# Optimization experiments

Measured on AMD Instinct MI355X. Metric: run time of the kernel, lower is better.

## Reference

```python
import jax, jax.numpy as jnp
import numpy as np

B, Q, NCLS1, C = 8, 900, 11, 256
NUM_ANCHOR = 100
H, W = 200, 200


def _make_view(b):
    # maps homogeneous (x0, y0, x1, y1, 1) box coords (meters-ish) to BEV pixels:
    # pixel = 20 * coord + 100  (keeps random boxes inside the 200x200 grid)
    v = np.zeros((5, 5), dtype=np.float32)
    for i in range(4):
        v[i, i] = 20.0
        v[i, 4] = 100.0
    v[4, 4] = 1.0
    return jnp.asarray(np.broadcast_to(v, (b, 5, 5)).copy())


def setup_inputs() -> dict:
    key = jax.random.key(0)
    k1, k2, k3 = jax.random.split(key, 3)
    return {
        "pred_boxes": jax.random.normal(k1, (B, Q, 4), dtype=jnp.float32),
        "pred_logits": jax.random.normal(k2, (B, Q, NCLS1), dtype=jnp.float32),
        "box_feats": jax.random.normal(k3, (B, Q, C), dtype=jnp.float32),
        "view": _make_view(B),
    }


def _box_to_bev(pred_boxes, pred_logits, box_feats, view):
    # scores = max over non-background classes of softmax(logits)
    scores = jnp.max(jax.nn.softmax(pred_logits, axis=-1)[..., :-1], axis=-1)  # [b,Q]
    _, idx = jax.lax.top_k(scores, NUM_ANCHOR)                                 # [b,N]

    boxes = jnp.take_along_axis(pred_boxes, idx[:, :, None], axis=1)[..., :4]  # [b,N,4]
    feats = jnp.take_along_axis(box_feats, idx[:, :, None], axis=1)            # [b,N,C]

    cx, cy = boxes[..., 0], boxes[..., 1]
    w, h = jnp.exp(boxes[..., 2]), jnp.exp(boxes[..., 3])
    xyxy = jnp.stack([cx - 0.5 * w, cy - 0.5 * h, cx + 0.5 * w, cy + 0.5 * h], axis=-1)
    xyxy1 = jnp.concatenate([xyxy, jnp.ones_like(xyxy[..., :1])], axis=-1)     # [b,N,5]

    coords = jnp.einsum("bij,bnj->bni", view, xyxy1)[..., :4].astype(jnp.int32)
    x0 = jnp.clip(coords[..., 0], 0, W)
    y0 = jnp.clip(coords[..., 1], 0, H)
    x1 = jnp.clip(coords[..., 2], 0, W)
    y1 = jnp.clip(coords[..., 3], 0, H)

    ys = jnp.arange(H, dtype=jnp.int32)
    xs = jnp.arange(W, dtype=jnp.int32)
    row = (ys[None, None, :] >= y0[:, :, None]) & (ys[None, None, :] < y1[:, :, None])  # [b,N,H]
    col = (xs[None, None, :] >= x0[:, :, None]) & (xs[None, None, :] < x1[:, :, None])  # [b,N,W]
    region = row[:, :, :, None] & col[:, :, None, :]                                    # [b,N,H,W]

    bev = jnp.einsum("bnhw,bnc->bhwc", region.astype(feats.dtype), feats)  # [b,H,W,C]
    mask = jnp.any(region, axis=1)                                          # [b,H,W]
    return bev, mask


def reference(pred_boxes, pred_logits, box_feats, view):
    return _box_to_bev(pred_boxes, pred_logits, box_feats, view)
```

## Files before the change

### kernel.cpp

```cpp
#include <hip/hip_runtime.h>
#include <math.h>

#define B_    8
#define Q_    900
#define NCLS_ 11
#define NANC_ 100
#define H_    200
#define W_    200
#define C_    256
#define HHALF 100
#define CHNK_ 113
#define CHEV_ 16

typedef float f32x4_ __attribute__((ext_vector_type(4)));

__global__ __launch_bounds__(128) void segdet_topk_kernel(
    const float* __restrict__ pred_boxes,
    const float* __restrict__ pred_logits,
    const float* __restrict__ view,
    int*  __restrict__ ws_idx,
    int4* __restrict__ ws_box)
{
    const int b     = blockIdx.x >> 3;
    const int chunk = blockIdx.x & 7;
    const int tid   = threadIdx.x;

    __shared__ __align__(16) float sc[Q_];

    for (int q2 = tid; q2 < Q_; q2 += 128) {
        const float* l = pred_logits + (b * Q_ + q2) * NCLS_;
        float v[NCLS_];
        float m = -INFINITY;
        #pragma unroll
        for (int i = 0; i < NCLS_; ++i) { v[i] = l[i]; m = fmaxf(m, v[i]); }
        float s = 0.0f, e10 = -INFINITY;
        #pragma unroll
        for (int i = 0; i < NCLS_; ++i) {
            float e = expf(v[i] - m);
            s += e;
            if (i < NCLS_ - 1) e10 = fmaxf(e10, e);
        }
        sc[q2] = e10 / s;
    }
    __syncthreads();

    const int q = chunk * CHNK_ + tid;
    if (tid < CHNK_ && q < Q_) {
        const float my = sc[q];
        int rank = 0;
        #pragma unroll 4
        for (int j4 = 0; j4 < Q_ / 4; ++j4) {
            const float4 o = *(const float4*)&sc[j4 * 4];
            const int j = j4 * 4;
            rank += (o.x > my) || (o.x == my && (j + 0) < q);
            rank += (o.y > my) || (o.y == my && (j + 1) < q);
            rank += (o.z > my) || (o.z == my && (j + 2) < q);
            rank += (o.w > my) || (o.w == my && (j + 3) < q);
        }
        if (rank < NANC_) {
            const float* bx = pred_boxes + (b * Q_ + q) * 4;
            double cx = (double)bx[0], cy = (double)bx[1];
            double w  = exp((double)bx[2]);
            double h  = exp((double)bx[3]);
            double p[5] = { cx - 0.5 * w, cy - 0.5 * h,
                            cx + 0.5 * w, cy + 0.5 * h, 1.0 };
            const float* v5 = view + b * 25;
            int ico[4];
            #pragma unroll
            for (int i = 0; i < 4; ++i) {
                double acc = 0.0;
                #pragma unroll
                for (int j = 0; j < 5; ++j) acc += (double)v5[i * 5 + j] * p[j];
                ico[i] = (int)acc;
            }
            int x0 = min(max(ico[0], 0), W_);
            int y0 = min(max(ico[1], 0), H_);
            int x1 = min(max(ico[2], 0), W_);
            int y1 = min(max(ico[3], 0), H_);
            const int slot = b * NANC_ + rank;
            ws_idx[slot] = q;
            ws_box[slot] = make_int4(x0, y0, x1, y1);
        }
    }
}

__device__ __forceinline__ void nt_store4(float* p, f32x4_ v) {
    __builtin_nontemporal_store(v, (f32x4_*)p);
}

__device__ __forceinline__ void gload_lds_16(const float* g, float* l) {
    __builtin_amdgcn_global_load_lds(
        (const __attribute__((address_space(1))) void*)g,
        (__attribute__((address_space(3))) void*)l,
        16, 0, 0);
}

__global__ __launch_bounds__(256) void segdet_bev_kernel(
    const float* __restrict__ box_feats,
    const int*   __restrict__ ws_idx,
    const int4*  __restrict__ ws_box,
    float* __restrict__ bev,
    float* __restrict__ mask)
{
    const int hidx = blockIdx.x / B_;
    const int b    = blockIdx.x % B_;
    const int h    = (hidx & 1) ? (HHALF - 1 - (hidx >> 1)) : (HHALF + (hidx >> 1));

    const int tid = threadIdx.x;
    const int ln  = tid & 63;
    const int wv  = tid >> 6;

    __shared__ __align__(16) float s_chunk[2][CHEV_ * C_];
    __shared__ int s_box[NANC_];
    __shared__ int s_nact;
    __shared__ int s_nopen[W_];
    __shared__ int s_ofs[W_ + 1];
    __shared__ int s_ent[2 * NANC_];
    __shared__ int s_wsum[4];

    if (tid < 64) {
        int na = 0;
        #pragma unroll
        for (int it = 0; it < 2; ++it) {
            int k = it * 64 + ln;
            bool act = false;
            int packed = 0;
            if (k < NANC_) {
                int4 bx = ws_box[b * NANC_ + k];
                int qi  = ws_idx[b * NANC_ + k];
                act = (bx.y <= h) && (h < bx.w) && (bx.x < bx.z);
                packed = bx.x | (bx.z << 8) | (qi << 16);
            }
            unsigned long long ball = __ballot(act);
            int pos = na + (int)__popcll(ball & ((1ull << ln) - 1ull));
            if (act) s_box[pos] = packed;
            na += (int)__popcll(ball);
        }
        if (ln == 0) s_nact = na;
    }
    __syncthreads();

    const int nact = s_nact;
    float* obase = bev + (size_t)(b * H_ + h) * W_ * C_ + ln * 4;
    float* mrow  = mask + (size_t)(b * H_ + h) * W_;

    if (nact == 0) {
        const f32x4_ z = {0.f, 0.f, 0.f, 0.f};
        for (int w = wv; w < W_; w += 4)
            nt_store4(obase + (size_t)w * C_, z);
        if (tid < W_) __builtin_nontemporal_store(0.0f, &mrow[tid]);
        return;
    }

    int ntot = 0;
    if (tid < W_) {
        int nopen = 0, nclose = 0, cov = 0;
        for (int k = 0; k < nact; ++k) {
            int pk = s_box[k];
            int x0 = pk & 0xFF, x1 = (pk >> 8) & 0xFF;
            nopen  += (x0 == tid);
            nclose += (x1 == tid);
            cov    += (x0 <= tid) && (tid < x1);
        }
        s_nopen[tid] = nopen;
        ntot = nopen + nclose;
        __builtin_nontemporal_store((cov > 0) ? 1.0f : 0.0f, &mrow[tid]);
    }

    int incl = ntot;
    #pragma unroll
    for (int d = 1; d < 64; d <<= 1) {
        int u = __shfl_up(incl, d);
        incl = (ln >= d) ? incl + u : incl;
    }
    if (ln == 63) s_wsum[wv] = incl;
    __syncthreads();

    int prev = 0;
    #pragma unroll
    for (int j = 0; j < 4; ++j) prev += (j < wv) ? s_wsum[j] : 0;
    const int ne = s_wsum[0] + s_wsum[1] + s_wsum[2] + s_wsum[3];
    if (tid < W_) s_ofs[tid] = prev + incl - ntot;
    if (tid == 0) s_ofs[W_] = ne;
    __syncthreads();

    if (tid < nact) {
        int pk = s_box[tid];
        int x0 = pk & 0xFF, x1 = (pk >> 8) & 0xFF, q = pk >> 16;
        int ro = 0, rc = 0;
        for (int j = 0; j < tid; ++j) {
            int pj = s_box[j];
            ro += ((pj & 0xFF) == x0);
            rc += (((pj >> 8) & 0xFF) == x1);
        }
        s_ent[s_ofs[x0] + ro] = q | (x0 << 10);
        if (x1 < W_)
            s_ent[s_ofs[x1] + s_nopen[x1] + rc] =
                (int)((unsigned)q | ((unsigned)x1 << 10) | 0x80000000u);
    }
    __syncthreads();

    const float* fbase = box_feats + (size_t)b * Q_ * C_ + ln * 4;
    const int nchunk = (ne + CHEV_ - 1) / CHEV_;

#define STAGE_(CI)                                                            \
    {                                                                         \
        const int base_ = (CI) * CHEV_;                                       \
        float* dst_ = &s_chunk[(CI) & 1][0];                                  \
        _Pragma("unroll")                                                     \
        for (int j = 0; j < 4; ++j) {                                         \
            const int e_ = base_ + wv * 4 + j;                                \
            if (e_ < ne) {                                                    \
                const int q_ = s_ent[e_] & 0x3FF;                             \
                gload_lds_16(fbase + (size_t)q_ * C_,                         \
                             dst_ + (wv * 4 + j) * C_);                       \
            }                                                                 \
        }                                                                     \
    }

    STAGE_(0);
    __syncthreads();

    f32x4_ acc = {0.f, 0.f, 0.f, 0.f};
    int cnt = 0;
    int w = wv;
    for (int ci = 0; ci < nchunk; ++ci) {
        if (ci + 1 < nchunk) STAGE_(ci + 1);
        const int ebeg = ci * CHEV_;
        const int eend = (ne < ebeg + CHEV_) ? ne : (ebeg + CHEV_);
        const float* cb = &s_chunk[ci & 1][0];
        for (int e = ebeg; e < eend; ++e) {
            const int ent = s_ent[e];
            const int pe  = (ent >> 10) & 0xFF;
            for (; w < pe; w += 4)
                nt_store4(obase + (size_t)w * C_, acc);
            const f32x4_ f = *(const f32x4_*)&cb[(e - ebeg) * C_ + ln * 4];
            if (ent < 0) { acc -= f; --cnt; }
            else         { acc += f; ++cnt; }
            if (cnt == 0) acc = (f32x4_){0.f, 0.f, 0.f, 0.f};
        }
        __syncthreads();
    }
#undef STAGE_
    for (; w < W_; w += 4)
        nt_store4(obase + (size_t)w * C_, acc);
}

extern "C" void kernel_launch(void* const* d_in, const int* in_sizes, int n_in,
                              void* d_out, int out_size, void* d_ws, size_t ws_size,
                              hipStream_t stream) {
    const float* pred_boxes  = (const float*)d_in[0];
    const float* pred_logits = (const float*)d_in[1];
    const float* box_feats   = (const float*)d_in[2];
    const float* view        = (const float*)d_in[3];

    float* bev  = (float*)d_out;
    float* mask = bev + (size_t)B_ * H_ * W_ * C_;

    int*  ws_idx = (int*)d_ws;
    int4* ws_box = (int4*)((char*)d_ws + 3200);

    segdet_topk_kernel<<<B_ * 8, 128, 0, stream>>>(pred_boxes, pred_logits, view,
                                                   ws_idx, ws_box);
    segdet_bev_kernel<<<B_ * H_, 256, 0, stream>>>(box_feats, ws_idx, ws_box,
                                                   bev, mask);
}
```

Measured before the change: 101.0 us.

## Split per-row event building into a separate prep kernel before BEV accumulation

```diff
diff --git a/kernel.cpp b/kernel.cpp
--- a/kernel.cpp
+++ b/kernel.cpp
@@ -11,6 +11,7 @@
 #define HHALF 100
 #define CHNK_ 113
 #define CHEV_ 16
+#define EVSTR_ 224
 
 typedef float f32x4_ __attribute__((ext_vector_type(4)));
 
@@ -95,6 +96,174 @@
         16, 0, 0);
 }
 
+__global__ __launch_bounds__(1024) void segdet_prep_kernel(
+    const int*  __restrict__ ws_idx,
+    const int4* __restrict__ ws_box,
+    int*  __restrict__ g_hdr,
+    int*  __restrict__ g_ev,
+    float* __restrict__ mask)
+{
+    const int sub = threadIdx.x >> 8;
+    const int t   = threadIdx.x & 255;
+    const int ln  = threadIdx.x & 63;
+    const int wv2 = (threadIdx.x >> 6) & 3;
+    const int rid = blockIdx.x * 4 + sub;
+    const int b   = rid / H_;
+    const int h   = rid % H_;
+
+    __shared__ __align__(16) int s_box[4][104];
+    __shared__ int s_na[4];
+    __shared__ int s_ws[4][4];
+
+    if (wv2 == 0) {
+        int na = 0;
+        #pragma unroll
+        for (int it = 0; it < 2; ++it) {
+            int k = it * 64 + ln;
+            bool act = false; int packed = 0;
+            if (k < NANC_) {
+                int4 bx = ws_box[b * NANC_ + k];
+                int qi  = ws_idx[b * NANC_ + k];
+                act = (bx.y <= h) && (h < bx.w) && (bx.x < bx.z);
+                packed = bx.x | (bx.z << 8) | (qi << 16);
+            }
+            unsigned long long ball = __ballot(act);
+            int pos = na + (int)__popcll(ball & ((1ull << ln) - 1ull));
+            if (act) s_box[sub][pos] = packed;
+            na += (int)__popcll(ball);
+        }
+        for (int idx = na + ln; idx < 104; idx += 64)
+            s_box[sub][idx] = 0xFFFF;
+        if (ln == 0) s_na[sub] = na;
+    }
+    __syncthreads();
+
+    const int nact = s_na[sub];
+    const int nk4  = (nact + 3) >> 2;
+
+    int nopen = 0, ncl = 0, cov = 0;
+#define CNT1_(PK) { const int x0_ = (PK) & 0xFF, x1_ = ((PK) >> 8) & 0xFF;    \
+        nopen += (x0_ == t); ncl += (x1_ == t);                               \
+        cov   += (x0_ <= t) && (t < x1_); }
+    if (t < W_) {
+        for (int k4 = 0; k4 < nk4; ++k4) {
+            const int4 p4 = *(const int4*)&s_box[sub][k4 * 4];
+            CNT1_(p4.x); CNT1_(p4.y); CNT1_(p4.z); CNT1_(p4.w);
+        }
+        mask[(size_t)rid * W_ + t] = (cov > 0) ? 1.0f : 0.0f;
+    }
+#undef CNT1_
+    const int ntot = nopen + ncl;
+
+    int incl = ntot;
+    #pragma unroll
+    for (int d = 1; d < 64; d <<= 1) {
+        int u = __shfl_up(incl, d);
+        incl = (ln >= d) ? incl + u : incl;
+    }
+    if (ln == 63) s_ws[sub][wv2] = incl;
+    __syncthreads();
+
+    int prev = 0;
+    #pragma unroll
+    for (int j = 0; j < 4; ++j) prev += (j < wv2) ? s_ws[sub][j] : 0;
+    const int ne  = s_ws[sub][0] + s_ws[sub][1] + s_ws[sub][2] + s_ws[sub][3];
+    const int ofs = prev + incl - ntot;
+    if (t == 0) g_hdr[rid] = ne;
+
+    if (t < W_ && ntot > 0) {
+        int po = ofs, pc = ofs + nopen;
+        int* dst = g_ev + (size_t)rid * EVSTR_;
+#define SCT1_(PK) { const int x0_ = (PK) & 0xFF, x1_ = ((PK) >> 8) & 0xFF;    \
+        const int q_ = (PK) >> 16;                                            \
+        if (x0_ == t) dst[po++] = q_ | (t << 10);                             \
+        if (x1_ == t) dst[pc++] = (int)((unsigned)q_ | ((unsigned)t << 10)    \
+                                         | 0x80000000u); }
+        for (int k4 = 0; k4 < nk4; ++k4) {
+            const int4 p4 = *(const int4*)&s_box[sub][k4 * 4];
+            SCT1_(p4.x); SCT1_(p4.y); SCT1_(p4.z); SCT1_(p4.w);
+        }
+#undef SCT1_
+    }
+}
+
+__global__ __launch_bounds__(256) void segdet_bev2_kernel(
+    const float* __restrict__ box_feats,
+    const int*   __restrict__ g_hdr,
+    const int*   __restrict__ g_ev,
+    float* __restrict__ bev)
+{
+    const int hidx = blockIdx.x / B_;
+    const int b    = blockIdx.x % B_;
+    const int h    = (hidx & 1) ? (HHALF - 1 - (hidx >> 1)) : (HHALF + (hidx >> 1));
+    const int rid  = b * H_ + h;
+
+    const int tid = threadIdx.x;
+    const int ln  = tid & 63;
+    const int wv  = tid >> 6;
+
+    __shared__ __align__(16) float s_chunk[2][CHEV_ * C_];
+    __shared__ int s_e[EVSTR_];
+
+    const int ne = g_hdr[rid];
+    float* obase = bev + (size_t)rid * W_ * C_ + ln * 4;
+
+    if (ne == 0) {
+        const f32x4_ z = {0.f, 0.f, 0.f, 0.f};
+        for (int w = wv; w < W_; w += 4)
+            nt_store4(obase + (size_t)w * C_, z);
+        return;
+    }
+
+    if (tid < EVSTR_) s_e[tid] = g_ev[(size_t)rid * EVSTR_ + tid];
+    __syncthreads();
+
+    const float* fbase = box_feats + (size_t)b * Q_ * C_ + ln * 4;
+    const int nchunk = (ne + CHEV_ - 1) / CHEV_;
+
+#define STAGE_(CI)                                                            \
+    {                                                                         \
+        const int base_ = (CI) * CHEV_;                                       \
+        float* dst_ = &s_chunk[(CI) & 1][0];                                  \
+        _Pragma("unroll")                                                     \
+        for (int j = 0; j < 4; ++j) {                                         \
+            const int e_ = base_ + wv * 4 + j;                                \
+            if (e_ < ne) {                                                    \
+                const int q_ = s_e[e_] & 0x3FF;                               \
+                gload_lds_16(fbase + (size_t)q_ * C_,                         \
+                             dst_ + (wv * 4 + j) * C_);                       \
+            }                                                                 \
+        }                                                                     \
+    }
+
+    STAGE_(0);
+    __syncthreads();
+
+    f32x4_ acc = {0.f, 0.f, 0.f, 0.f};
+    int cnt = 0;
+    int w = wv;
+    for (int ci = 0; ci < nchunk; ++ci) {
+        if (ci + 1 < nchunk) STAGE_(ci + 1);
+        const int ebeg = ci * CHEV_;
+        const int eend = (ne < ebeg + CHEV_) ? ne : (ebeg + CHEV_);
+        const float* cb = &s_chunk[ci & 1][0];
+        for (int e = ebeg; e < eend; ++e) {
+            const int ent = s_e[e];
+            const int pe  = (ent >> 10) & 0xFF;
+            for (; w < pe; w += 4)
+                nt_store4(obase + (size_t)w * C_, acc);
+            const f32x4_ f = *(const f32x4_*)&cb[(e - ebeg) * C_ + ln * 4];
+            if (ent < 0) { acc -= f; --cnt; }
+            else         { acc += f; ++cnt; }
+            if (cnt == 0) acc = (f32x4_){0.f, 0.f, 0.f, 0.f};
+        }
+        __syncthreads();
+    }
+#undef STAGE_
+    for (; w < W_; w += 4)
+        nt_store4(obase + (size_t)w * C_, acc);
+}
+
 __global__ __launch_bounds__(256) void segdet_bev_kernel(
     const float* __restrict__ box_feats,
     const int*   __restrict__ ws_idx,
@@ -259,9 +428,19 @@
 
     int*  ws_idx = (int*)d_ws;
     int4* ws_box = (int4*)((char*)d_ws + 3200);
+    int*  g_hdr  = (int*)((char*)d_ws + 16000);
+    int*  g_ev   = (int*)((char*)d_ws + 22400);
+    const size_t need = 22400ull + (size_t)B_ * H_ * EVSTR_ * 4ull;
 
     segdet_topk_kernel<<<B_ * 8, 128, 0, stream>>>(pred_boxes, pred_logits, view,
                                                    ws_idx, ws_box);
-    segdet_bev_kernel<<<B_ * H_, 256, 0, stream>>>(box_feats, ws_idx, ws_box,
-                                                   bev, mask);
-}
+    if (ws_size >= need) {
+        segdet_prep_kernel<<<(B_ * H_) / 4, 1024, 0, stream>>>(
+            ws_idx, ws_box, g_hdr, g_ev, mask);
+        segdet_bev2_kernel<<<B_ * H_, 256, 0, stream>>>(
+            box_feats, g_hdr, g_ev, bev);
+    } else {
+        segdet_bev_kernel<<<B_ * H_, 256, 0, stream>>>(
+            box_feats, ws_idx, ws_box, bev, mask);
+    }
+}
```

After: 113.7 us. +12.5%, slower.
